# Performance work log

Hardware: AMD Instinct MI355X
Metric: run time of the kernel (lower is better)

## Reference

```python
import jax, jax.numpy as jnp
import numpy as np

B, LQ, LK, D, H = 4, 2048, 2048, 1024, 16
HD = D // H  # head dim = 64


def setup_inputs() -> dict:
    key = jax.random.key(0)
    ks = jax.random.split(key, 8)
    s = 1.0 / np.sqrt(D)
    return {
        "zt": jax.random.normal(ks[0], (B, LQ, D), jnp.float32),
        "ic": jax.random.normal(ks[1], (B, LK, D), jnp.float32),
        "Wq": jax.random.normal(ks[2], (D, D), jnp.float32) * s,
        "bq": jax.random.normal(ks[3], (D,), jnp.float32) * 0.01,
        "Wk": jax.random.normal(ks[4], (D, D), jnp.float32) * s,
        "bk": jax.random.normal(ks[5], (D,), jnp.float32) * 0.01,
        "Wv": jax.random.normal(ks[6], (D, D), jnp.float32) * s,
        "bv": jax.random.normal(ks[7], (D,), jnp.float32) * 0.01,
    }


def reference(zt, ic, Wq, bq, Wk, bk, Wv, bv):
    # Linear projections (torch Linear: x @ W.T + b); weights here stored as [out, in]
    q = zt @ Wq.T + bq            # [B, LQ, D]
    k = ic @ Wk.T + bk            # [B, LK, D]
    v = ic @ Wv.T + bv            # [B, LK, D]
    # split heads -> [B, H, L, HD]
    q = q.reshape(B, LQ, H, HD).transpose(0, 2, 1, 3)
    k = k.reshape(B, LK, H, HD).transpose(0, 2, 1, 3)
    v = v.reshape(B, LK, H, HD).transpose(0, 2, 1, 3)
    scale = 1.0 / jnp.sqrt(jnp.asarray(HD, q.dtype))
    scores = jnp.einsum('bhqd,bhkd->bhqk', q, k) * scale  # [B, H, LQ, LK]
    attn = jax.nn.softmax(scores, axis=-1)
    out = jnp.einsum('bhqk,bhkd->bhqd', attn, v)          # [B, H, LQ, HD]
    return out.transpose(0, 2, 1, 3).reshape(B, LQ, D)
```

## Files before the change

kernel.cpp:

```cpp
#include <hip/hip_runtime.h>
#include <hip/hip_bf16.h>
#include <cstdint>

#define B_  4
#define LQ_ 2048
#define LK_ 2048
#define D_  1024
#define H_  16
#define HD_ 64

typedef __attribute__((ext_vector_type(8))) short bf16x8;
typedef __attribute__((ext_vector_type(4))) float f32x4;

#if defined(__has_builtin)
#if __has_builtin(__builtin_amdgcn_exp2f)
#define EXP2F(x) __builtin_amdgcn_exp2f(x)
#else
#define EXP2F(x) exp2f(x)
#endif
#else
#define EXP2F(x) exp2f(x)
#endif

__device__ __forceinline__ unsigned short f2b(float f) {
    union { float f; unsigned u; } v; v.f = f;
    unsigned u = v.u;
    unsigned r = (u + 0x7fffu + ((u >> 16) & 1u)) >> 16;
    return (unsigned short)r;
}

__device__ __forceinline__ void gl_lds16(const unsigned short* g, unsigned short* l) {
    __builtin_amdgcn_global_load_lds(
        (const __attribute__((address_space(1))) unsigned int*)(g),
        (__attribute__((address_space(3))) unsigned int*)(l),
        16, 0, 0);
}

#define PHASE_BARRIER() do { \
    __builtin_amdgcn_sched_barrier(0); \
    __builtin_amdgcn_s_barrier(); \
    __builtin_amdgcn_sched_barrier(0); } while (0)

#define WAITVM(N) do { \
    asm volatile("s_waitcnt vmcnt(" #N ")" ::: "memory"); \
    __builtin_amdgcn_sched_barrier(0); } while (0)

__global__ void cvt_all(const float* __restrict__ a0, unsigned short* __restrict__ d0,
                        const float* __restrict__ a1, unsigned short* __restrict__ d1,
                        const float* __restrict__ w0, unsigned short* __restrict__ e0, float s0,
                        const float* __restrict__ w1, unsigned short* __restrict__ e1,
                        const float* __restrict__ w2, unsigned short* __restrict__ e2,
                        int nact, int nw) {
    const float* in; unsigned short* out; float s = 1.0f; int n;
    switch (blockIdx.y) {
        case 0: in = a0; out = d0; n = nact; break;
        case 1: in = a1; out = d1; n = nact; break;
        case 2: in = w0; out = e0; n = nw; s = s0; break;
        case 3: in = w1; out = e1; n = nw; break;
        default: in = w2; out = e2; n = nw; break;
    }
    int i = (blockIdx.x * blockDim.x + threadIdx.x) * 8;
    int stride = gridDim.x * blockDim.x * 8;
    for (; i < n; i += stride) {
        float4 x = *(const float4*)(in + i);
        float4 y = *(const float4*)(in + i + 4);
        bf16x8 v;
        v[0] = (short)f2b(x.x * s); v[1] = (short)f2b(x.y * s);
        v[2] = (short)f2b(x.z * s); v[3] = (short)f2b(x.w * s);
        v[4] = (short)f2b(y.x * s); v[5] = (short)f2b(y.y * s);
        v[6] = (short)f2b(y.z * s); v[7] = (short)f2b(y.w * s);
        *(bf16x8*)(out + i) = v;
    }
}

__global__ __launch_bounds__(512, 2) void qkv_gemm(
    const unsigned short* __restrict__ Xq,
    const unsigned short* __restrict__ Xkv,
    const unsigned short* __restrict__ Wqb, const unsigned short* __restrict__ Wkb,
    const unsigned short* __restrict__ Wvb,
    const float* __restrict__ bq, const float* __restrict__ bk,
    const float* __restrict__ bv, float qscale,
    unsigned short* __restrict__ Qb, unsigned short* __restrict__ Kb,
    unsigned short* __restrict__ Vb)
{
    __shared__ unsigned short AS[4][8192];
    __shared__ unsigned short BS[4][8192];

    const int proj = blockIdx.y >> 2;
    const int nt0  = blockIdx.y & 3;
    const unsigned short* X = (proj == 0) ? Xq : Xkv;
    const unsigned short* W = (proj == 0) ? Wqb : (proj == 1 ? Wkb : Wvb);
    const float* bias       = (proj == 0) ? bq  : (proj == 1 ? bk  : bv);
    unsigned short* Y       = (proj == 0) ? Qb  : (proj == 1 ? Kb  : Vb);
    const float bscale      = (proj == 0) ? qscale : 1.0f;

    const int tid  = threadIdx.x;
    const int lane = tid & 63;
    const int w    = tid >> 6;
    const int wm   = w & 1, wn = w >> 1;
    const int m0   = blockIdx.x * 256;
    const int n0   = nt0 * 256;
    const int l15  = lane & 15, quad = lane >> 4;

    f32x4 acc[8][4] = {};

    const unsigned short* gA0 = X + (size_t)(m0 + (w * 2) * 16 + l15) * 1024 + quad * 8;
    const unsigned short* gA1 = gA0 + 16 * 1024;
    const unsigned short* gB0 = W + (size_t)(n0 + (w * 2) * 16 + l15) * 1024 + quad * 8;
    const unsigned short* gB1 = gB0 + 16 * 1024;

#define STAGE_A(slot, koff) do { \
    gl_lds16(gA0 + (koff), &AS[slot][(w * 2) * 512 + lane * 8]); \
    gl_lds16(gA1 + (koff), &AS[slot][(w * 2 + 1) * 512 + lane * 8]); } while (0)
#define STAGE_B(slot, koff) do { \
    gl_lds16(gB0 + (koff), &BS[slot][(w * 2) * 512 + lane * 8]); \
    gl_lds16(gB1 + (koff), &BS[slot][(w * 2 + 1) * 512 + lane * 8]); } while (0)

    const int aoff = (wm * 8) * 512 + lane * 8;
    const int boff = (wn * 4) * 512 + lane * 8;

    STAGE_A(0, 0);   STAGE_B(0, 0);
    STAGE_A(1, 32);  STAGE_B(1, 32);
    STAGE_A(2, 64);  STAGE_B(2, 64);
    WAITVM(8);
    __builtin_amdgcn_s_barrier();
    __builtin_amdgcn_sched_barrier(0);

    #pragma unroll 2
    for (int t = 0; t < 16; ++t) {
        const int s0 = (2 * t) & 3;
        const int s1 = (2 * t + 1) & 3;
        const int s3 = (2 * t + 3) & 3;

        bf16x8 af[8], bf0, bf1;

        #pragma unroll
        for (int i = 0; i < 8; ++i)
            af[i] = *(const bf16x8*)(&AS[s0][aoff + i * 512]);
        bf0 = *(const bf16x8*)(&BS[s0][boff]);
        bf1 = *(const bf16x8*)(&BS[s0][boff + 512]);
        PHASE_BARRIER();
        __builtin_amdgcn_s_setprio(1);
        #pragma unroll
        for (int i = 0; i < 8; ++i) {
            acc[i][0] = __builtin_amdgcn_mfma_f32_16x16x32_bf16(af[i], bf0, acc[i][0], 0, 0, 0);
            acc[i][1] = __builtin_amdgcn_mfma_f32_16x16x32_bf16(af[i], bf1, acc[i][1], 0, 0, 0);
        }
        __builtin_amdgcn_s_setprio(0);
        if (t < 15) STAGE_A(s3, (t + 1) * 64 + 32);

        bf0 = *(const bf16x8*)(&BS[s0][boff + 1024]);
        bf1 = *(const bf16x8*)(&BS[s0][boff + 1536]);
        if (t < 14) { WAITVM(6); } else { WAITVM(0); }
        PHASE_BARRIER();
        __builtin_amdgcn_s_setprio(1);
        #pragma unroll
        for (int i = 0; i < 8; ++i) {
            acc[i][2] = __builtin_amdgcn_mfma_f32_16x16x32_bf16(af[i], bf0, acc[i][2], 0, 0, 0);
            acc[i][3] = __builtin_amdgcn_mfma_f32_16x16x32_bf16(af[i], bf1, acc[i][3], 0, 0, 0);
        }
        __builtin_amdgcn_s_setprio(0);
        if (t < 15) STAGE_B(s3, (t + 1) * 64 + 32);

        #pragma unroll
        for (int i = 0; i < 8; ++i)
            af[i] = *(const bf16x8*)(&AS[s1][aoff + i * 512]);
        bf0 = *(const bf16x8*)(&BS[s1][boff]);
        bf1 = *(const bf16x8*)(&BS[s1][boff + 512]);
        PHASE_BARRIER();
        __builtin_amdgcn_s_setprio(1);
        #pragma unroll
        for (int i = 0; i < 8; ++i) {
            acc[i][0] = __builtin_amdgcn_mfma_f32_16x16x32_bf16(af[i], bf0, acc[i][0], 0, 0, 0);
            acc[i][1] = __builtin_amdgcn_mfma_f32_16x16x32_bf16(af[i], bf1, acc[i][1], 0, 0, 0);
        }
        __builtin_amdgcn_s_setprio(0);
        if (t < 14) STAGE_A(s0, (t + 2) * 64);

        bf0 = *(const bf16x8*)(&BS[s1][boff + 1024]);
        bf1 = *(const bf16x8*)(&BS[s1][boff + 1536]);
        if (t < 14) { WAITVM(6); } else if (t == 14) { WAITVM(4); }
        PHASE_BARRIER();
        __builtin_amdgcn_s_setprio(1);
        #pragma unroll
        for (int i = 0; i < 8; ++i) {
            acc[i][2] = __builtin_amdgcn_mfma_f32_16x16x32_bf16(af[i], bf0, acc[i][2], 0, 0, 0);
            acc[i][3] = __builtin_amdgcn_mfma_f32_16x16x32_bf16(af[i], bf1, acc[i][3], 0, 0, 0);
        }
        __builtin_amdgcn_s_setprio(0);
        if (t < 14) STAGE_B(s0, (t + 2) * 64);
    }

#undef STAGE_A
#undef STAGE_B

    float bvv[4];
    #pragma unroll
    for (int j = 0; j < 4; ++j)
        bvv[j] = bias[n0 + wn * 64 + j * 16 + l15] * bscale;

    #pragma unroll
    for (int i = 0; i < 8; ++i) {
        #pragma unroll
        for (int r = 0; r < 4; ++r) {
            int row = m0 + wm * 128 + i * 16 + quad * 4 + r;
            unsigned short* yp = Y + (size_t)row * 1024 + n0 + wn * 64;
            #pragma unroll
            for (int j = 0; j < 4; ++j)
                yp[j * 16 + l15] = f2b(acc[i][j][r] + bvv[j]);
        }
    }
}

__global__ __launch_bounds__(256) void transpose_v(
    const unsigned short* __restrict__ Vb, unsigned short* __restrict__ Vt)
{
    __shared__ unsigned short L[64 * 72];
    const int t0 = blockIdx.x * 64, h = blockIdx.y, b = blockIdx.z;
    const int rr = threadIdx.x >> 3;
    const int cc = (threadIdx.x & 7) * 8;

    #pragma unroll
    for (int p = 0; p < 2; ++p) {
        int r = rr + p * 32;
        *(bf16x8*)(&L[r * 72 + cc]) =
            *(const bf16x8*)(Vb + (size_t)(b * 2048 + t0 + r) * 1024 + h * 64 + cc);
    }
    __syncthreads();
    #pragma unroll
    for (int p = 0; p < 2; ++p) {
        int d = rr + p * 32;
        bf16x8 v;
        #pragma unroll
        for (int j = 0; j < 8; ++j)
            v[j] = (short)L[(cc + j) * 72 + d];
        *(bf16x8*)(Vt + ((size_t)(b * 16 + h) * 64 + d) * 2048 + t0 + cc) = v;
    }
}

__global__ __launch_bounds__(256, 2) void attn_kernel(
    const unsigned short* __restrict__ Q,
    const unsigned short* __restrict__ Kp,
    const unsigned short* __restrict__ Vt,
    float* __restrict__ Out)
{
    __shared__ unsigned short Ks[2][16 * 512];
    __shared__ unsigned short Vs[16 * 512];
    __shared__ unsigned short Ps[4][4096];

    const int tid  = threadIdx.x;
    const int lane = tid & 63;
    const int w    = tid >> 6;
    const int l15  = lane & 15, quad = lane >> 4;

    const int bid = blockIdx.x + (blockIdx.y << 3) + (blockIdx.z << 7);
    const int glo = bid & 7;
    const int jx  = bid >> 3;
    const int qt  = jx & 7;
    const int g   = glo + ((jx >> 3) << 3);
    const int h   = g & 15;
    const int b   = g >> 4;

    bf16x8 qf[4][2];
    #pragma unroll
    for (int half = 0; half < 4; ++half) {
        const unsigned short* qptr =
            Q + (size_t)(b * LQ_ + qt * 256 + w * 64 + half * 16 + l15) * 1024 + h * 64;
        qf[half][0] = *(const bf16x8*)(qptr + quad * 8);
        qf[half][1] = *(const bf16x8*)(qptr + 32 + quad * 8);
    }

    bf16x8 ones;
    #pragma unroll
    for (int j = 0; j < 8; ++j) ones[j] = (short)0x3F80;

    f32x4 oacc[4][4] = {};
    f32x4 lacc[4]    = {};

    const unsigned short* Kbase = Kp + (size_t)b * LK_ * 1024 + h * 64;
    const unsigned short* Vbase = Vt + (size_t)(b * 16 + h) * 64 * 2048;

    const unsigned short* gK[4];
    unsigned short* lK[4];
    const unsigned short* gV[4];
    unsigned short* lV[4];
    #pragma unroll
    for (int j = 0; j < 4; ++j) {
        int kt = w + (j >> 1) * 4, dblk = j & 1;
        gK[j] = Kbase + (size_t)(kt * 16 + l15) * 1024 + dblk * 32 + quad * 8;
        lK[j] = &Ks[0][(kt * 2 + dblk) * 512 + lane * 8];
        gV[j] = Vbase + (size_t)(w * 16 + l15) * 2048 + j * 32 + quad * 8;
        lV[j] = &Vs[(w * 4 + j) * 512 + lane * 8];
    }

    const int pws = (quad >> 1) * 128 + l15 * 8 + (quad & 1) * 4;
    unsigned short* PwB = &Ps[w][pws];
    const unsigned short* PrB = &Ps[w][lane * 8];
    const unsigned short* KfrB = &Ks[0][lane * 8];
    const unsigned short* Vfr = &Vs[lane * 8];

    #pragma unroll
    for (int j = 0; j < 4; ++j) gl_lds16(gK[j], lK[j]);

    for (int t = 0; t < 16; ++t) {
        const int cur = t & 1;
        const int k0 = t * 128;

        #pragma unroll
        for (int j = 0; j < 4; ++j) gl_lds16(gV[j] + k0, lV[j]);
        if (t < 15) {
            const int stoff = (cur ^ 1) * 8192;
            #pragma unroll
            for (int j = 0; j < 4; ++j)
                gl_lds16(gK[j] + (size_t)(t + 1) * (128 * 1024), lK[j] + stoff);
        }
        if (t == 0) {
            WAITVM(8);
            PHASE_BARRIER();
        }
        const unsigned short* Kfr = KfrB + cur * 8192;

        #pragma unroll
        for (int cc = 0; cc < 2; ++cc) {
            f32x4 st[4][4] = {};
            #pragma unroll
            for (int ti = 0; ti < 4; ++ti)
                #pragma unroll
                for (int dblk = 0; dblk < 2; ++dblk) {
                    bf16x8 kf = *(const bf16x8*)(Kfr + ((cc * 4 + ti) * 2 + dblk) * 512);
                    #pragma unroll
                    for (int half = 0; half < 4; ++half)
                        st[half][ti] = __builtin_amdgcn_mfma_f32_16x16x32_bf16(
                            kf, qf[half][dblk], st[half][ti], 0, 0, 0);
                }

            #pragma unroll
            for (int half = 0; half < 4; ++half) {
                unsigned short* pw = PwB + half * 1024;
                #pragma unroll
                for (int ti = 0; ti < 4; ++ti) {
                    unsigned u0 = __float_as_uint(EXP2F(st[half][ti][0])) + 0x8000u;
                    unsigned u1 = __float_as_uint(EXP2F(st[half][ti][1])) + 0x8000u;
                    unsigned u2 = __float_as_uint(EXP2F(st[half][ti][2])) + 0x8000u;
                    unsigned u3 = __float_as_uint(EXP2F(st[half][ti][3])) + 0x8000u;
                    uint2 pk;
                    pk.x = __builtin_amdgcn_perm(u1, u0, 0x07060302);
                    pk.y = __builtin_amdgcn_perm(u3, u2, 0x07060302);
                    *(uint2*)(pw + ti * 256) = pk;
                }
            }

            if (cc == 0) {
                if (t < 15) { WAITVM(4); } else { WAITVM(0); }
                PHASE_BARRIER();
            }

            #pragma unroll
            for (int hbl = 0; hbl < 2; ++hbl) {
                bf16x8 pf[4];
                #pragma unroll
                for (int half = 0; half < 4; ++half) {
                    pf[half] = *(const bf16x8*)(PrB + half * 1024 + hbl * 512);
                    lacc[half] = __builtin_amdgcn_mfma_f32_16x16x32_bf16(
                        pf[half], ones, lacc[half], 0, 0, 0);
                }
                int hb = cc * 2 + hbl;
                #pragma unroll
                for (int nt = 0; nt < 4; ++nt) {
                    bf16x8 vf = *(const bf16x8*)(Vfr + (nt * 4 + hb) * 512);
                    #pragma unroll
                    for (int half = 0; half < 4; ++half)
                        oacc[half][nt] = __builtin_amdgcn_mfma_f32_16x16x32_bf16(
                            pf[half], vf, oacc[half][nt], 0, 0, 0);
                }
            }
        }

        if (t < 15) {
            WAITVM(0);
            PHASE_BARRIER();
        }
    }

    #pragma unroll
    for (int half = 0; half < 4; ++half) {
        float il[4];
        #pragma unroll
        for (int r = 0; r < 4; ++r) il[r] = 1.0f / lacc[half][r];
        #pragma unroll
        for (int nt = 0; nt < 4; ++nt) {
            #pragma unroll
            for (int r = 0; r < 4; ++r) {
                size_t orow = (size_t)(b * LQ_ + qt * 256 + w * 64 + half * 16 + quad * 4 + r);
                Out[orow * 1024 + h * 64 + nt * 16 + l15] = oacc[half][nt][r] * il[r];
            }
        }
    }
}

extern "C" void kernel_launch(void* const* d_in, const int* in_sizes, int n_in,
                              void* d_out, int out_size, void* d_ws, size_t ws_size,
                              hipStream_t stream) {
    const float* zt = (const float*)d_in[0];
    const float* ic = (const float*)d_in[1];
    const float* Wq = (const float*)d_in[2];
    const float* bq = (const float*)d_in[3];
    const float* Wk = (const float*)d_in[4];
    const float* bk = (const float*)d_in[5];
    const float* Wv = (const float*)d_in[6];
    const float* bv = (const float*)d_in[7];
    float* out = (float*)d_out;

    const size_t M8 = (size_t)8192 * 1024;
    const size_t M1 = (size_t)1024 * 1024;
    unsigned short* Qb  = (unsigned short*)d_ws;
    unsigned short* Kb  = Qb  + M8;
    unsigned short* Vb  = Kb  + M8;
    unsigned short* Xz  = Vb  + M8;
    unsigned short* Xi  = Xz  + M8;
    unsigned short* Wqb = Xi  + M8;
    unsigned short* Wkb = Wqb + M1;
    unsigned short* Wvb = Wkb + M1;
    unsigned short* Vtb = Xz;

    const float qscale = 0.125f * 1.44269504088896f;

    dim3 gcv(4096, 5);
    cvt_all<<<gcv, 256, 0, stream>>>(zt, Xz, ic, Xi,
                                     Wq, Wqb, qscale, Wk, Wkb, Wv, Wvb,
                                     (int)M8, (int)M1);

    dim3 gproj(32, 12);
    qkv_gemm<<<gproj, 512, 0, stream>>>(Xz, Xi, Wqb, Wkb, Wvb,
                                        bq, bk, bv, qscale, Qb, Kb, Vb);

    dim3 gtr(32, 16, 4);
    transpose_v<<<gtr, 256, 0, stream>>>(Vb, Vtb);

    dim3 gattn(8, 16, 4);
    attn_kernel<<<gattn, 256, 0, stream>>>(Qb, Kb, Vtb, out);
}
```

Measured before the change: 295.5 us.

## Shrink QKV GEMM tiles to 128x128 with XCD-aware block mapping

Changes the QKV projection GEMM from 256x256 tiles with 512 threads to 128x128 tiles with 256 threads. The grid goes from 384 to 1536 blocks, and a 1D block index is remapped so each XCD handles contiguous M-tiles for better L2 locality. The aim is to fill the CUs better and reduce tail effects. In exchange, each block reuses less data per tile, so global and LDS traffic per FLOP rises.

```diff
diff --git a/kernel.cpp b/kernel.cpp
--- a/kernel.cpp
+++ b/kernel.cpp
@@ -73,7 +73,7 @@
     }
 }
 
-__global__ __launch_bounds__(512, 2) void qkv_gemm(
+__global__ __launch_bounds__(256, 2) void qkv_gemm(
     const unsigned short* __restrict__ Xq,
     const unsigned short* __restrict__ Xkv,
     const unsigned short* __restrict__ Wqb, const unsigned short* __restrict__ Wkb,
@@ -83,11 +83,17 @@
     unsigned short* __restrict__ Qb, unsigned short* __restrict__ Kb,
     unsigned short* __restrict__ Vb)
 {
-    __shared__ unsigned short AS[4][8192];
-    __shared__ unsigned short BS[4][8192];
-
-    const int proj = blockIdx.y >> 2;
-    const int nt0  = blockIdx.y & 3;
+    __shared__ unsigned short AS[4][4096];
+    __shared__ unsigned short BS[4][4096];
+
+    const int bid  = blockIdx.x;
+    const int xcd  = bid & 7;
+    const int idx  = bid >> 3;
+    const int mt   = xcd * 8 + (idx & 7);
+    const int yy   = idx >> 3;
+    const int proj = yy >> 3;
+    const int nt0  = yy & 7;
+
     const unsigned short* X = (proj == 0) ? Xq : Xkv;
     const unsigned short* W = (proj == 0) ? Wqb : (proj == 1 ? Wkb : Wvb);
     const float* bias       = (proj == 0) ? bq  : (proj == 1 ? bk  : bv);
@@ -98,25 +104,25 @@
     const int lane = tid & 63;
     const int w    = tid >> 6;
     const int wm   = w & 1, wn = w >> 1;
-    const int m0   = blockIdx.x * 256;
-    const int n0   = nt0 * 256;
+    const int m0   = mt * 128;
+    const int n0   = nt0 * 128;
     const int l15  = lane & 15, quad = lane >> 4;
 
-    f32x4 acc[8][4] = {};
-
-    const unsigned short* gA0 = X + (size_t)(m0 + (w * 2) * 16 + l15) * 1024 + quad * 8;
-    const unsigned short* gA1 = gA0 + 16 * 1024;
-    const unsigned short* gB0 = W + (size_t)(n0 + (w * 2) * 16 + l15) * 1024 + quad * 8;
-    const unsigned short* gB1 = gB0 + 16 * 1024;
+    f32x4 acc[4][4] = {};
+
+    const unsigned short* gA0 = X + (size_t)(m0 + w * 16 + l15) * 1024 + quad * 8;
+    const unsigned short* gA1 = gA0 + 4 * 16 * 1024;
+    const unsigned short* gB0 = W + (size_t)(n0 + w * 16 + l15) * 1024 + quad * 8;
+    const unsigned short* gB1 = gB0 + 4 * 16 * 1024;
 
 #define STAGE_A(slot, koff) do { \
-    gl_lds16(gA0 + (koff), &AS[slot][(w * 2) * 512 + lane * 8]); \
-    gl_lds16(gA1 + (koff), &AS[slot][(w * 2 + 1) * 512 + lane * 8]); } while (0)
+    gl_lds16(gA0 + (koff), &AS[slot][w * 512 + lane * 8]); \
+    gl_lds16(gA1 + (koff), &AS[slot][(w + 4) * 512 + lane * 8]); } while (0)
 #define STAGE_B(slot, koff) do { \
-    gl_lds16(gB0 + (koff), &BS[slot][(w * 2) * 512 + lane * 8]); \
-    gl_lds16(gB1 + (koff), &BS[slot][(w * 2 + 1) * 512 + lane * 8]); } while (0)
-
-    const int aoff = (wm * 8) * 512 + lane * 8;
+    gl_lds16(gB0 + (koff), &BS[slot][w * 512 + lane * 8]); \
+    gl_lds16(gB1 + (koff), &BS[slot][(w + 4) * 512 + lane * 8]); } while (0)
+
+    const int aoff = (wm * 4) * 512 + lane * 8;
     const int boff = (wn * 4) * 512 + lane * 8;
 
     STAGE_A(0, 0);   STAGE_B(0, 0);
@@ -132,17 +138,17 @@
         const int s1 = (2 * t + 1) & 3;
         const int s3 = (2 * t + 3) & 3;
 
-        bf16x8 af[8], bf0, bf1;
-
-        #pragma unroll
-        for (int i = 0; i < 8; ++i)
+        bf16x8 af[4], bf0, bf1;
+
+        #pragma unroll
+        for (int i = 0; i < 4; ++i)
             af[i] = *(const bf16x8*)(&AS[s0][aoff + i * 512]);
         bf0 = *(const bf16x8*)(&BS[s0][boff]);
         bf1 = *(const bf16x8*)(&BS[s0][boff + 512]);
         PHASE_BARRIER();
         __builtin_amdgcn_s_setprio(1);
         #pragma unroll
-        for (int i = 0; i < 8; ++i) {
+        for (int i = 0; i < 4; ++i) {
             acc[i][0] = __builtin_amdgcn_mfma_f32_16x16x32_bf16(af[i], bf0, acc[i][0], 0, 0, 0);
             acc[i][1] = __builtin_amdgcn_mfma_f32_16x16x32_bf16(af[i], bf1, acc[i][1], 0, 0, 0);
         }
@@ -155,7 +161,7 @@
         PHASE_BARRIER();
         __builtin_amdgcn_s_setprio(1);
         #pragma unroll
-        for (int i = 0; i < 8; ++i) {
+        for (int i = 0; i < 4; ++i) {
             acc[i][2] = __builtin_amdgcn_mfma_f32_16x16x32_bf16(af[i], bf0, acc[i][2], 0, 0, 0);
             acc[i][3] = __builtin_amdgcn_mfma_f32_16x16x32_bf16(af[i], bf1, acc[i][3], 0, 0, 0);
         }
@@ -163,14 +169,14 @@
         if (t < 15) STAGE_B(s3, (t + 1) * 64 + 32);
 
         #pragma unroll
-        for (int i = 0; i < 8; ++i)
+        for (int i = 0; i < 4; ++i)
             af[i] = *(const bf16x8*)(&AS[s1][aoff + i * 512]);
         bf0 = *(const bf16x8*)(&BS[s1][boff]);
         bf1 = *(const bf16x8*)(&BS[s1][boff + 512]);
         PHASE_BARRIER();
         __builtin_amdgcn_s_setprio(1);
         #pragma unroll
-        for (int i = 0; i < 8; ++i) {
+        for (int i = 0; i < 4; ++i) {
             acc[i][0] = __builtin_amdgcn_mfma_f32_16x16x32_bf16(af[i], bf0, acc[i][0], 0, 0, 0);
             acc[i][1] = __builtin_amdgcn_mfma_f32_16x16x32_bf16(af[i], bf1, acc[i][1], 0, 0, 0);
         }
@@ -183,7 +189,7 @@
         PHASE_BARRIER();
         __builtin_amdgcn_s_setprio(1);
         #pragma unroll
-        for (int i = 0; i < 8; ++i) {
+        for (int i = 0; i < 4; ++i) {
             acc[i][2] = __builtin_amdgcn_mfma_f32_16x16x32_bf16(af[i], bf0, acc[i][2], 0, 0, 0);
             acc[i][3] = __builtin_amdgcn_mfma_f32_16x16x32_bf16(af[i], bf1, acc[i][3], 0, 0, 0);
         }
@@ -200,10 +206,10 @@
         bvv[j] = bias[n0 + wn * 64 + j * 16 + l15] * bscale;
 
     #pragma unroll
-    for (int i = 0; i < 8; ++i) {
+    for (int i = 0; i < 4; ++i) {
         #pragma unroll
         for (int r = 0; r < 4; ++r) {
-            int row = m0 + wm * 128 + i * 16 + quad * 4 + r;
+            int row = m0 + wm * 64 + i * 16 + quad * 4 + r;
             unsigned short* yp = Y + (size_t)row * 1024 + n0 + wn * 64;
             #pragma unroll
             for (int j = 0; j < 4; ++j)
@@ -430,9 +436,8 @@
                                      Wq, Wqb, qscale, Wk, Wkb, Wv, Wvb,
                                      (int)M8, (int)M1);
 
-    dim3 gproj(32, 12);
-    qkv_gemm<<<gproj, 512, 0, stream>>>(Xz, Xi, Wqb, Wkb, Wvb,
-                                        bq, bk, bv, qscale, Qb, Kb, Vb);
+    qkv_gemm<<<dim3(1536), 256, 0, stream>>>(Xz, Xi, Wqb, Wkb, Wvb,
+                                             bq, bk, bv, qscale, Qb, Kb, Vb);
 
     dim3 gtr(32, 16, 4);
     transpose_v<<<gtr, 256, 0, stream>>>(Vb, Vtb);
```

Result: slower. 310.9 us (+5.2%).

## Keep softmax probabilities in registers, using 16x16x16 MFMA for PV

Applied to the files above, without the earlier changes.

Drops the per-wave LDS staging buffer for the probability matrix. The bf16-packed exp values are fed straight from registers into 16x16x16 MFMAs, using the score accumulator layout as the A operand, and V fragments are read from LDS with matching 4-element offsets. This removes LDS writes, reads and the shared footprint for P, which could raise occupancy. In exchange it doubles the number of MFMA instructions, each with half the K depth, and issues more, narrower V loads.

```diff
diff --git a/kernel.cpp b/kernel.cpp
--- a/kernel.cpp
+++ b/kernel.cpp
@@ -10,6 +10,7 @@
 #define HD_ 64
 
 typedef __attribute__((ext_vector_type(8))) short bf16x8;
+typedef __attribute__((ext_vector_type(4))) short bf16x4;
 typedef __attribute__((ext_vector_type(4))) float f32x4;
 
 #if defined(__has_builtin)
@@ -246,7 +247,6 @@
 {
     __shared__ unsigned short Ks[2][16 * 512];
     __shared__ unsigned short Vs[16 * 512];
-    __shared__ unsigned short Ps[4][4096];
 
     const int tid  = threadIdx.x;
     const int lane = tid & 63;
@@ -270,9 +270,9 @@
         qf[half][1] = *(const bf16x8*)(qptr + 32 + quad * 8);
     }
 
-    bf16x8 ones;
-    #pragma unroll
-    for (int j = 0; j < 8; ++j) ones[j] = (short)0x3F80;
+    bf16x4 ones4;
+    #pragma unroll
+    for (int j = 0; j < 4; ++j) ones4[j] = (short)0x3F80;
 
     f32x4 oacc[4][4] = {};
     f32x4 lacc[4]    = {};
@@ -293,11 +293,8 @@
         lV[j] = &Vs[(w * 4 + j) * 512 + lane * 8];
     }
 
-    const int pws = (quad >> 1) * 128 + l15 * 8 + (quad & 1) * 4;
-    unsigned short* PwB = &Ps[w][pws];
-    const unsigned short* PrB = &Ps[w][lane * 8];
     const unsigned short* KfrB = &Ks[0][lane * 8];
-    const unsigned short* Vfr = &Vs[lane * 8];
+    const unsigned short* VfrB = &Vs[(quad >> 1) * 128 + l15 * 8 + (quad & 1) * 4];
 
     #pragma unroll
     for (int j = 0; j < 4; ++j) gl_lds16(gK[j], lK[j]);
@@ -334,21 +331,20 @@
                             kf, qf[half][dblk], st[half][ti], 0, 0, 0);
                 }
 
-            #pragma unroll
-            for (int half = 0; half < 4; ++half) {
-                unsigned short* pw = PwB + half * 1024;
+            bf16x4 pf[4][4];
+            #pragma unroll
+            for (int half = 0; half < 4; ++half)
                 #pragma unroll
                 for (int ti = 0; ti < 4; ++ti) {
                     unsigned u0 = __float_as_uint(EXP2F(st[half][ti][0])) + 0x8000u;
                     unsigned u1 = __float_as_uint(EXP2F(st[half][ti][1])) + 0x8000u;
                     unsigned u2 = __float_as_uint(EXP2F(st[half][ti][2])) + 0x8000u;
                     unsigned u3 = __float_as_uint(EXP2F(st[half][ti][3])) + 0x8000u;
-                    uint2 pk;
-                    pk.x = __builtin_amdgcn_perm(u1, u0, 0x07060302);
-                    pk.y = __builtin_amdgcn_perm(u3, u2, 0x07060302);
-                    *(uint2*)(pw + ti * 256) = pk;
+                    union { uint2 u; bf16x4 b; } cv;
+                    cv.u.x = __builtin_amdgcn_perm(u1, u0, 0x07060302);
+                    cv.u.y = __builtin_amdgcn_perm(u3, u2, 0x07060302);
+                    pf[half][ti] = cv.b;
                 }
-            }
 
             if (cc == 0) {
                 if (t < 15) { WAITVM(4); } else { WAITVM(0); }
@@ -356,22 +352,21 @@
             }
 
             #pragma unroll
-            for (int hbl = 0; hbl < 2; ++hbl) {
-                bf16x8 pf[4];
+            for (int ti = 0; ti < 4; ++ti) {
+                const int s = cc * 4 + ti;
+                const unsigned short* vb = VfrB + (s >> 1) * 512 + (s & 1) * 256;
+                bf16x4 vf[4];
+                #pragma unroll
+                for (int nt = 0; nt < 4; ++nt)
+                    vf[nt] = *(const bf16x4*)(vb + nt * 2048);
                 #pragma unroll
                 for (int half = 0; half < 4; ++half) {
-                    pf[half] = *(const bf16x8*)(PrB + half * 1024 + hbl * 512);
-                    lacc[half] = __builtin_amdgcn_mfma_f32_16x16x32_bf16(
-                        pf[half], ones, lacc[half], 0, 0, 0);
-                }
-                int hb = cc * 2 + hbl;
-                #pragma unroll
-                for (int nt = 0; nt < 4; ++nt) {
-                    bf16x8 vf = *(const bf16x8*)(Vfr + (nt * 4 + hb) * 512);
+                    lacc[half] = __builtin_amdgcn_mfma_f32_16x16x16bf16_1k(
+                        pf[half][ti], ones4, lacc[half], 0, 0, 0);
                     #pragma unroll
-                    for (int half = 0; half < 4; ++half)
-                        oacc[half][nt] = __builtin_amdgcn_mfma_f32_16x16x32_bf16(
-                            pf[half], vf, oacc[half][nt], 0, 0, 0);
+                    for (int nt = 0; nt < 4; ++nt)
+                        oacc[half][nt] = __builtin_amdgcn_mfma_f32_16x16x16bf16_1k(
+                            pf[half][ti], vf[nt], oacc[half][nt], 0, 0, 0);
                 }
             }
         }
```

Result: slower. 307.9 us (+4.2%).
